# Kernel optimization log

Measured on AMD Instinct MI355X. Metric: run time of the kernel, lower is better.

The kernel has to match this reference:

```python
import jax, jax.numpy as jnp
import numpy as np

B, D, L, O = 131072, 128, 4, 1  # batch, d_model, num_layers(depths), estimator out dim


def setup_inputs() -> dict:
    key = jax.random.key(0)
    k0, k1, k2, k3 = jax.random.split(key, 4)
    x = jax.random.normal(k0, (B, D), jnp.float32)
    Wr = jax.random.normal(k1, (D, L), jnp.float32) * (1.0 / np.sqrt(D))
    W_layers = jax.random.normal(k2, (L, 2 * D, D), jnp.float32) * (1.0 / np.sqrt(2 * D))
    b_layers = jnp.zeros((L, D), jnp.float32)
    W_est = jax.random.normal(k3, (L, D, O), jnp.float32) * (1.0 / np.sqrt(D))
    b_est = jnp.zeros((L, O), jnp.float32)
    return {"x": x, "Wr": Wr, "W_layers": W_layers, "b_layers": b_layers,
            "W_est": W_est, "b_est": b_est}


def reference(x, Wr, W_layers, b_layers, W_est, b_est):
    # Router on stop_gradient(inputs); ReLU gate -> genuinely sparse gates (>0 test).
    gates = jax.nn.relu(jax.lax.stop_gradient(x) @ Wr)  # [B, L]

    def compute(last_out, depth):
        # layer depth: Dense on [last_layer_output, init_input]
        cur = jax.nn.relu(
            jnp.concatenate([last_out, x], axis=-1) @ W_layers[depth] + b_layers[depth]
        )  # [B, D]
        preds = cur @ W_est[depth] + b_est[depth]  # estimator at this depth, [B, O]
        if depth == L - 1:
            return preds
        # SparseDispatcher2D over 2 experts (exit / enter). combine() is an
        # unsorted_segment_sum over tokens with gate > 0 (unweighted), which is
        # exactly a 0/1-mask sum per token -- dense, jit-friendly equivalent.
        mask_exit = (gates[:, depth] > 0.0).astype(cur.dtype)[:, None]
        mask_enter = (jnp.sum(gates[:, depth + 1:], axis=1) > 0.0).astype(cur.dtype)[:, None]
        return mask_exit * preds + mask_enter * compute(cur, depth + 1)

    return compute(x, 0)
```

## Files before the change

### kernel.cpp

```cpp
#include <hip/hip_runtime.h>
#include <cstddef>

typedef float f4 __attribute__((ext_vector_type(4)));
typedef __bf16 bf16x8 __attribute__((ext_vector_type(8)));
typedef __bf16 bf16x4 __attribute__((ext_vector_type(4)));
typedef float f32x16 __attribute__((ext_vector_type(16)));

constexpr int D_ = 128;
constexpr int LAYERS = 4;
constexpr int BM = 128;
constexpr int NT = 256;
constexpr int ROWB = 512;

__device__ __forceinline__ int swz(int row, int woff) {
    return row * ROWB + (woff ^ ((row & 15) << 4));
}

__global__ void prep(const float* __restrict__ Wl, __bf16* __restrict__ wt2) {
    int idx = blockIdx.x * 256 + threadIdx.x;
    int j = idx & 7, lane = (idx >> 3) & 63, kc = (idx >> 9) & 15,
        nf = (idx >> 13) & 3, d = idx >> 15;
    int n  = nf * 32 + (lane & 31);
    int ks = kc * 16 + (lane >> 5) * 8 + j;
    float v;
    if (d == 0)
        v = (ks < 128) ? 0.f
                       : (Wl[(size_t)(ks - 128) * D_ + n] + Wl[(size_t)ks * D_ + n]);
    else
        v = Wl[(size_t)d * 2 * D_ * D_ + (size_t)ks * D_ + n];
    wt2[idx] = (__bf16)v;
}

__global__ __launch_bounds__(NT, 2)
void moe_fwd(const float* __restrict__ x, const float* __restrict__ Wr,
             const __bf16* __restrict__ wt2, const float* __restrict__ bl,
             const float* __restrict__ We, const float* __restrict__ be,
             float* __restrict__ out)
{
    __shared__ char Ab[BM * ROWB];
    __shared__ float PR[2][BM];
    __shared__ float CSM[BM][4];

    const int t    = threadIdx.x;
    const int m0   = blockIdx.x * BM;
    const int lane = t & 63, w = t >> 6;
    const int nw   = w >> 1;
    const int tw   = w & 1;
    const int lo5  = lane & 31, hi = lane >> 5;
    const int hi16 = hi * 16;
    const int tok0 = tw * 64 + lo5, tok1 = tok0 + 32;
    const int grp  = t >> 4, il = t & 15;

    f4 wrv[8];
    #pragma unroll
    for (int j = 0; j < 8; ++j)
        wrv[j] = *(const f4*)(Wr + (il * 8 + j) * 4);

    #pragma unroll
    for (int i = 0; i < 8; ++i) {
        const int row = i * 16 + grp;
        const f4* gx = (const f4*)(x + (size_t)(m0 + row) * D_ + il * 8);
        f4 lo = gx[0], hp = gx[1];
        bf16x8 v;
        v[0] = (__bf16)lo[0]; v[1] = (__bf16)lo[1]; v[2] = (__bf16)lo[2]; v[3] = (__bf16)lo[3];
        v[4] = (__bf16)hp[0]; v[5] = (__bf16)hp[1]; v[6] = (__bf16)hp[2]; v[7] = (__bf16)hp[3];
        *(bf16x8*)(Ab + swz(row, 256 + il * 16)) = v;

        double a0 = 0, a1 = 0, a2 = 0, a3 = 0;
        #pragma unroll
        for (int j = 0; j < 4; ++j) {
            double xv = (double)lo[j];
            a0 += xv * (double)wrv[j][0]; a1 += xv * (double)wrv[j][1];
            a2 += xv * (double)wrv[j][2]; a3 += xv * (double)wrv[j][3];
        }
        #pragma unroll
        for (int j = 0; j < 4; ++j) {
            double xv = (double)hp[j];
            a0 += xv * (double)wrv[4 + j][0]; a1 += xv * (double)wrv[4 + j][1];
            a2 += xv * (double)wrv[4 + j][2]; a3 += xv * (double)wrv[4 + j][3];
        }
        #pragma unroll
        for (int s = 1; s < 16; s <<= 1) {
            a0 += __shfl_xor(a0, s, 16);
            a1 += __shfl_xor(a1, s, 16);
            a2 += __shfl_xor(a2, s, 16);
            a3 += __shfl_xor(a3, s, 16);
        }
        if (il == 0) {
            f4 c;
            c[0] = a0 > 0.0 ? 1.f : 0.f; c[1] = a1 > 0.0 ? 1.f : 0.f;
            c[2] = a2 > 0.0 ? 1.f : 0.f; c[3] = a3 > 0.0 ? 1.f : 0.f;
            *(f4*)(&CSM[row][0]) = c;
        }
    }

    float outc = 0.f;
    __syncthreads();

    #pragma unroll
    for (int d = 0; d < LAYERS; ++d) {
        const int kstart = (d == 0) ? 8 : 0;

        bf16x8 wf[2][16];
        {
            const __bf16* wb = wt2 + ((size_t)(d * 4 + nw * 2) * 16) * 512 + lane * 8;
            #pragma unroll
            for (int m = 0; m < 2; ++m)
                #pragma unroll
                for (int kc = 0; kc < 16; ++kc)
                    if (kc >= kstart)
                        wf[m][kc] = *(const bf16x8*)(wb + (size_t)(m * 16 + kc) * 512);
        }

        f32x16 acc[2][2];
        #pragma unroll
        for (int m = 0; m < 2; ++m)
            #pragma unroll
            for (int tf = 0; tf < 2; ++tf)
                #pragma unroll
                for (int j = 0; j < 16; ++j) acc[m][tf][j] = 0.f;

        #pragma unroll
        for (int ks = 0; ks < 16; ++ks) {
            if (ks < kstart) continue;
            int wo = ks * 32 + hi16;
            bf16x8 b0 = *(const bf16x8*)(Ab + swz(tok0, wo));
            bf16x8 b1 = *(const bf16x8*)(Ab + swz(tok1, wo));
            acc[0][0] = __builtin_amdgcn_mfma_f32_32x32x16_bf16(wf[0][ks], b0, acc[0][0], 0, 0, 0);
            acc[0][1] = __builtin_amdgcn_mfma_f32_32x32x16_bf16(wf[0][ks], b1, acc[0][1], 0, 0, 0);
            acc[1][0] = __builtin_amdgcn_mfma_f32_32x32x16_bf16(wf[1][ks], b0, acc[1][0], 0, 0, 0);
            acc[1][1] = __builtin_amdgcn_mfma_f32_32x32x16_bf16(wf[1][ks], b1, acc[1][1], 0, 0, 0);
        }
        __syncthreads();

        float p0 = 0.f, p1 = 0.f;
        #pragma unroll
        for (int m = 0; m < 2; ++m) {
            #pragma unroll
            for (int rg = 0; rg < 4; ++rg) {
                int nb = nw * 64 + m * 32 + rg * 8 + hi * 4;
                f4 bv = *(const f4*)(bl + d * D_ + nb);
                f4 ev = *(const f4*)(We + d * D_ + nb);
                #pragma unroll
                for (int tf = 0; tf < 2; ++tf) {
                    float c0 = fmaxf(acc[m][tf][rg * 4 + 0] + bv[0], 0.f);
                    float c1 = fmaxf(acc[m][tf][rg * 4 + 1] + bv[1], 0.f);
                    float c2 = fmaxf(acc[m][tf][rg * 4 + 2] + bv[2], 0.f);
                    float c3 = fmaxf(acc[m][tf][rg * 4 + 3] + bv[3], 0.f);
                    float pp = c0 * ev[0] + c1 * ev[1] + c2 * ev[2] + c3 * ev[3];
                    if (tf == 0) p0 += pp; else p1 += pp;
                    if (d < LAYERS - 1) {
                        bf16x4 cc;
                        cc[0] = (__bf16)c0; cc[1] = (__bf16)c1;
                        cc[2] = (__bf16)c2; cc[3] = (__bf16)c3;
                        int token = tw * 64 + tf * 32 + lo5;
                        *(bf16x4*)(Ab + swz(token, nb * 2)) = cc;
                    }
                }
            }
        }
        p0 += __shfl_xor(p0, 32, 64);
        p1 += __shfl_xor(p1, 32, 64);
        if (lane < 32) {
            PR[nw][tw * 64 + lo5]      = p0;
            PR[nw][tw * 64 + 32 + lo5] = p1;
        }
        __syncthreads();

        if (t < BM)
            outc += CSM[t][d] * (PR[0][t] + PR[1][t] + be[d]);
    }

    if (t < BM) out[m0 + t] = outc;
}

extern "C" void kernel_launch(void* const* d_in, const int* in_sizes, int n_in,
                              void* d_out, int out_size, void* d_ws, size_t ws_size,
                              hipStream_t stream) {
    const float* x  = (const float*)d_in[0];
    const float* Wr = (const float*)d_in[1];
    const float* Wl = (const float*)d_in[2];
    const float* bl = (const float*)d_in[3];
    const float* We = (const float*)d_in[4];
    const float* be = (const float*)d_in[5];
    float* out = (float*)d_out;
    __bf16* wt2 = (__bf16*)d_ws;
    const int B = in_sizes[0] / D_;

    prep<<<dim3(512), dim3(256), 0, stream>>>(Wl, wt2);
    moe_fwd<<<dim3(B / BM), dim3(NT), 0, stream>>>(x, Wr, wt2, bl, We, be, out);
}
```

Before: 56.37 us.

## Double block threads to eight waves, each owning one 32-wide output slice

Raises the block from 256 to 512 threads so each of eight waves computes one 32-column output fragment for 64 tokens, instead of two fragments per wave. Each wave now holds half the weight registers and half the accumulators, which lowers register pressure and allows more concurrent waves. The initial x load and router loop is split across twice as many threads, and the partial estimator sums are reduced over four slices instead of two. Trade-offs are more threads contending at each barrier and more redundant LDS reads of the token operand.

```diff
diff --git a/kernel.cpp b/kernel.cpp
--- a/kernel.cpp
+++ b/kernel.cpp
@@ -9,7 +9,7 @@
 constexpr int D_ = 128;
 constexpr int LAYERS = 4;
 constexpr int BM = 128;
-constexpr int NT = 256;
+constexpr int NT = 512;
 constexpr int ROWB = 512;
 
 __device__ __forceinline__ int swz(int row, int woff) {
@@ -31,20 +31,20 @@
     wt2[idx] = (__bf16)v;
 }
 
-__global__ __launch_bounds__(NT, 2)
+__global__ __launch_bounds__(NT, 4)
 void moe_fwd(const float* __restrict__ x, const float* __restrict__ Wr,
              const __bf16* __restrict__ wt2, const float* __restrict__ bl,
              const float* __restrict__ We, const float* __restrict__ be,
              float* __restrict__ out)
 {
     __shared__ char Ab[BM * ROWB];
-    __shared__ float PR[2][BM];
+    __shared__ float PR[4][BM];
     __shared__ float CSM[BM][4];
 
     const int t    = threadIdx.x;
     const int m0   = blockIdx.x * BM;
     const int lane = t & 63, w = t >> 6;
-    const int nw   = w >> 1;
+    const int nf   = w >> 1;
     const int tw   = w & 1;
     const int lo5  = lane & 31, hi = lane >> 5;
     const int hi16 = hi * 16;
@@ -57,8 +57,8 @@
         wrv[j] = *(const f4*)(Wr + (il * 8 + j) * 4);
 
     #pragma unroll
-    for (int i = 0; i < 8; ++i) {
-        const int row = i * 16 + grp;
+    for (int i = 0; i < 4; ++i) {
+        const int row = i * 32 + grp;
         const f4* gx = (const f4*)(x + (size_t)(m0 + row) * D_ + il * 8);
         f4 lo = gx[0], hp = gx[1];
         bf16x8 v;
@@ -101,24 +101,20 @@
     for (int d = 0; d < LAYERS; ++d) {
         const int kstart = (d == 0) ? 8 : 0;
 
-        bf16x8 wf[2][16];
+        bf16x8 wf[16];
         {
-            const __bf16* wb = wt2 + ((size_t)(d * 4 + nw * 2) * 16) * 512 + lane * 8;
+            const __bf16* wb = wt2 + ((size_t)(d * 4 + nf) * 16) * 512 + lane * 8;
             #pragma unroll
-            for (int m = 0; m < 2; ++m)
-                #pragma unroll
-                for (int kc = 0; kc < 16; ++kc)
-                    if (kc >= kstart)
-                        wf[m][kc] = *(const bf16x8*)(wb + (size_t)(m * 16 + kc) * 512);
+            for (int kc = 0; kc < 16; ++kc)
+                if (kc >= kstart)
+                    wf[kc] = *(const bf16x8*)(wb + (size_t)kc * 512);
         }
 
-        f32x16 acc[2][2];
+        f32x16 acc[2];
         #pragma unroll
-        for (int m = 0; m < 2; ++m)
+        for (int tf = 0; tf < 2; ++tf)
             #pragma unroll
-            for (int tf = 0; tf < 2; ++tf)
-                #pragma unroll
-                for (int j = 0; j < 16; ++j) acc[m][tf][j] = 0.f;
+            for (int j = 0; j < 16; ++j) acc[tf][j] = 0.f;
 
         #pragma unroll
         for (int ks = 0; ks < 16; ++ks) {
@@ -126,49 +122,44 @@
             int wo = ks * 32 + hi16;
             bf16x8 b0 = *(const bf16x8*)(Ab + swz(tok0, wo));
             bf16x8 b1 = *(const bf16x8*)(Ab + swz(tok1, wo));
-            acc[0][0] = __builtin_amdgcn_mfma_f32_32x32x16_bf16(wf[0][ks], b0, acc[0][0], 0, 0, 0);
-            acc[0][1] = __builtin_amdgcn_mfma_f32_32x32x16_bf16(wf[0][ks], b1, acc[0][1], 0, 0, 0);
-            acc[1][0] = __builtin_amdgcn_mfma_f32_32x32x16_bf16(wf[1][ks], b0, acc[1][0], 0, 0, 0);
-            acc[1][1] = __builtin_amdgcn_mfma_f32_32x32x16_bf16(wf[1][ks], b1, acc[1][1], 0, 0, 0);
+            acc[0] = __builtin_amdgcn_mfma_f32_32x32x16_bf16(wf[ks], b0, acc[0], 0, 0, 0);
+            acc[1] = __builtin_amdgcn_mfma_f32_32x32x16_bf16(wf[ks], b1, acc[1], 0, 0, 0);
         }
         __syncthreads();
 
         float p0 = 0.f, p1 = 0.f;
         #pragma unroll
-        for (int m = 0; m < 2; ++m) {
+        for (int rg = 0; rg < 4; ++rg) {
+            int nb = nf * 32 + rg * 8 + hi * 4;
+            f4 bv = *(const f4*)(bl + d * D_ + nb);
+            f4 ev = *(const f4*)(We + d * D_ + nb);
             #pragma unroll
-            for (int rg = 0; rg < 4; ++rg) {
-                int nb = nw * 64 + m * 32 + rg * 8 + hi * 4;
-                f4 bv = *(const f4*)(bl + d * D_ + nb);
-                f4 ev = *(const f4*)(We + d * D_ + nb);
-                #pragma unroll
-                for (int tf = 0; tf < 2; ++tf) {
-                    float c0 = fmaxf(acc[m][tf][rg * 4 + 0] + bv[0], 0.f);
-                    float c1 = fmaxf(acc[m][tf][rg * 4 + 1] + bv[1], 0.f);
-                    float c2 = fmaxf(acc[m][tf][rg * 4 + 2] + bv[2], 0.f);
-                    float c3 = fmaxf(acc[m][tf][rg * 4 + 3] + bv[3], 0.f);
-                    float pp = c0 * ev[0] + c1 * ev[1] + c2 * ev[2] + c3 * ev[3];
-                    if (tf == 0) p0 += pp; else p1 += pp;
-                    if (d < LAYERS - 1) {
-                        bf16x4 cc;
-                        cc[0] = (__bf16)c0; cc[1] = (__bf16)c1;
-                        cc[2] = (__bf16)c2; cc[3] = (__bf16)c3;
-                        int token = tw * 64 + tf * 32 + lo5;
-                        *(bf16x4*)(Ab + swz(token, nb * 2)) = cc;
-                    }
+            for (int tf = 0; tf < 2; ++tf) {
+                float c0 = fmaxf(acc[tf][rg * 4 + 0] + bv[0], 0.f);
+                float c1 = fmaxf(acc[tf][rg * 4 + 1] + bv[1], 0.f);
+                float c2 = fmaxf(acc[tf][rg * 4 + 2] + bv[2], 0.f);
+                float c3 = fmaxf(acc[tf][rg * 4 + 3] + bv[3], 0.f);
+                float pp = c0 * ev[0] + c1 * ev[1] + c2 * ev[2] + c3 * ev[3];
+                if (tf == 0) p0 += pp; else p1 += pp;
+                if (d < LAYERS - 1) {
+                    bf16x4 cc;
+                    cc[0] = (__bf16)c0; cc[1] = (__bf16)c1;
+                    cc[2] = (__bf16)c2; cc[3] = (__bf16)c3;
+                    int token = tw * 64 + tf * 32 + lo5;
+                    *(bf16x4*)(Ab + swz(token, nb * 2)) = cc;
                 }
             }
         }
         p0 += __shfl_xor(p0, 32, 64);
         p1 += __shfl_xor(p1, 32, 64);
         if (lane < 32) {
-            PR[nw][tw * 64 + lo5]      = p0;
-            PR[nw][tw * 64 + 32 + lo5] = p1;
+            PR[nf][tw * 64 + lo5]      = p0;
+            PR[nf][tw * 64 + 32 + lo5] = p1;
         }
         __syncthreads();
 
         if (t < BM)
-            outc += CSM[t][d] * (PR[0][t] + PR[1][t] + be[d]);
+            outc += CSM[t][d] * (PR[0][t] + PR[1][t] + PR[2][t] + PR[3][t] + be[d]);
     }
 
     if (t < BM) out[m0 + t] = outc;
```

After: 54.27 us. -3.7%, faster.

## Keep activations in registers across layers via permuted weight K-order

Applied to the files above, without the earlier changes.

Each wave now owns 32 tokens and all 128 output columns, so the layer output produced in MFMA accumulator layout is repacked directly into registers as the next layer's B operand. The prep kernel permutes the K rows of layers 1-3 so that the register layout matches, which removes the shared-memory activation buffer and most block barriers. Shared memory drops to the gate table and launch bounds rise to 3 blocks per SM for occupancy. In exchange each wave loads the full weight set per layer (four times more weight traffic per wave), and register pressure rises from holding x and previous-layer activations.

```diff
diff --git a/kernel.cpp b/kernel.cpp
--- a/kernel.cpp
+++ b/kernel.cpp
@@ -3,175 +3,152 @@
 
 typedef float f4 __attribute__((ext_vector_type(4)));
 typedef __bf16 bf16x8 __attribute__((ext_vector_type(8)));
-typedef __bf16 bf16x4 __attribute__((ext_vector_type(4)));
 typedef float f32x16 __attribute__((ext_vector_type(16)));
 
 constexpr int D_ = 128;
 constexpr int LAYERS = 4;
 constexpr int BM = 128;
 constexpr int NT = 256;
-constexpr int ROWB = 512;
-
-__device__ __forceinline__ int swz(int row, int woff) {
-    return row * ROWB + (woff ^ ((row & 15) << 4));
-}
 
 __global__ void prep(const float* __restrict__ Wl, __bf16* __restrict__ wt2) {
     int idx = blockIdx.x * 256 + threadIdx.x;
-    int j = idx & 7, lane = (idx >> 3) & 63, kc = (idx >> 9) & 15,
-        nf = (idx >> 13) & 3, d = idx >> 15;
-    int n  = nf * 32 + (lane & 31);
-    int ks = kc * 16 + (lane >> 5) * 8 + j;
+    int j = idx & 7, lane = (idx >> 3) & 63, f = (idx >> 9) & 15,
+        c = (idx >> 13) & 3, d = idx >> 15;
+    int n = c * 32 + (lane & 31);
+    int k = f * 16 + (lane >> 5) * 8 + j;
     float v;
-    if (d == 0)
-        v = (ks < 128) ? 0.f
-                       : (Wl[(size_t)(ks - 128) * D_ + n] + Wl[(size_t)ks * D_ + n]);
-    else
-        v = Wl[(size_t)d * 2 * D_ * D_ + (size_t)ks * D_ + n];
+    if (d == 0) {
+        v = (k < 128) ? 0.f
+                      : (Wl[(size_t)(k - 128) * D_ + n] + Wl[(size_t)k * D_ + n]);
+    } else {
+        int kl;
+        if (k < 128) {
+            int jj = k & 7, hh = (k >> 3) & 1, ff = (k >> 4) & 7;
+            kl = (ff >> 1) * 32 + ((ff & 1) * 2 + (jj >> 2)) * 8 + hh * 4 + (jj & 3);
+        } else {
+            kl = k;
+        }
+        v = Wl[(size_t)d * 2 * D_ * D_ + (size_t)kl * D_ + n];
+    }
     wt2[idx] = (__bf16)v;
 }
 
-__global__ __launch_bounds__(NT, 2)
+__global__ __launch_bounds__(NT, 3)
 void moe_fwd(const float* __restrict__ x, const float* __restrict__ Wr,
              const __bf16* __restrict__ wt2, const float* __restrict__ bl,
              const float* __restrict__ We, const float* __restrict__ be,
              float* __restrict__ out)
 {
-    __shared__ char Ab[BM * ROWB];
-    __shared__ float PR[2][BM];
     __shared__ float CSM[BM][4];
 
     const int t    = threadIdx.x;
     const int m0   = blockIdx.x * BM;
     const int lane = t & 63, w = t >> 6;
-    const int nw   = w >> 1;
-    const int tw   = w & 1;
     const int lo5  = lane & 31, hi = lane >> 5;
-    const int hi16 = hi * 16;
-    const int tok0 = tw * 64 + lo5, tok1 = tok0 + 32;
+    const int tok  = w * 32 + lo5;
     const int grp  = t >> 4, il = t & 15;
 
-    f4 wrv[8];
+    bf16x8 xb[8];
     #pragma unroll
-    for (int j = 0; j < 8; ++j)
-        wrv[j] = *(const f4*)(Wr + (il * 8 + j) * 4);
+    for (int fi = 0; fi < 8; ++fi) {
+        const f4* gx = (const f4*)(x + (size_t)(m0 + tok) * D_ + fi * 16 + hi * 8);
+        f4 a = gx[0], b = gx[1];
+        xb[fi][0] = (__bf16)a[0]; xb[fi][1] = (__bf16)a[1];
+        xb[fi][2] = (__bf16)a[2]; xb[fi][3] = (__bf16)a[3];
+        xb[fi][4] = (__bf16)b[0]; xb[fi][5] = (__bf16)b[1];
+        xb[fi][6] = (__bf16)b[2]; xb[fi][7] = (__bf16)b[3];
+    }
 
-    #pragma unroll
-    for (int i = 0; i < 8; ++i) {
-        const int row = i * 16 + grp;
-        const f4* gx = (const f4*)(x + (size_t)(m0 + row) * D_ + il * 8);
-        f4 lo = gx[0], hp = gx[1];
-        bf16x8 v;
-        v[0] = (__bf16)lo[0]; v[1] = (__bf16)lo[1]; v[2] = (__bf16)lo[2]; v[3] = (__bf16)lo[3];
-        v[4] = (__bf16)hp[0]; v[5] = (__bf16)hp[1]; v[6] = (__bf16)hp[2]; v[7] = (__bf16)hp[3];
-        *(bf16x8*)(Ab + swz(row, 256 + il * 16)) = v;
-
-        double a0 = 0, a1 = 0, a2 = 0, a3 = 0;
+    {
+        f4 wrv[8];
         #pragma unroll
-        for (int j = 0; j < 4; ++j) {
-            double xv = (double)lo[j];
-            a0 += xv * (double)wrv[j][0]; a1 += xv * (double)wrv[j][1];
-            a2 += xv * (double)wrv[j][2]; a3 += xv * (double)wrv[j][3];
-        }
+        for (int j = 0; j < 8; ++j)
+            wrv[j] = *(const f4*)(Wr + (il * 8 + j) * 4);
         #pragma unroll
-        for (int j = 0; j < 4; ++j) {
-            double xv = (double)hp[j];
-            a0 += xv * (double)wrv[4 + j][0]; a1 += xv * (double)wrv[4 + j][1];
-            a2 += xv * (double)wrv[4 + j][2]; a3 += xv * (double)wrv[4 + j][3];
-        }
-        #pragma unroll
-        for (int s = 1; s < 16; s <<= 1) {
-            a0 += __shfl_xor(a0, s, 16);
-            a1 += __shfl_xor(a1, s, 16);
-            a2 += __shfl_xor(a2, s, 16);
-            a3 += __shfl_xor(a3, s, 16);
-        }
-        if (il == 0) {
-            f4 c;
-            c[0] = a0 > 0.0 ? 1.f : 0.f; c[1] = a1 > 0.0 ? 1.f : 0.f;
-            c[2] = a2 > 0.0 ? 1.f : 0.f; c[3] = a3 > 0.0 ? 1.f : 0.f;
-            *(f4*)(&CSM[row][0]) = c;
+        for (int i = 0; i < 8; ++i) {
+            const int row = i * 16 + grp;
+            const f4* gx = (const f4*)(x + (size_t)(m0 + row) * D_ + il * 8);
+            f4 lo = gx[0], hp = gx[1];
+            double a0 = 0, a1 = 0, a2 = 0, a3 = 0;
+            #pragma unroll
+            for (int j = 0; j < 4; ++j) {
+                double xv = (double)lo[j];
+                a0 += xv * (double)wrv[j][0]; a1 += xv * (double)wrv[j][1];
+                a2 += xv * (double)wrv[j][2]; a3 += xv * (double)wrv[j][3];
+            }
+            #pragma unroll
+            for (int j = 0; j < 4; ++j) {
+                double xv = (double)hp[j];
+                a0 += xv * (double)wrv[4 + j][0]; a1 += xv * (double)wrv[4 + j][1];
+                a2 += xv * (double)wrv[4 + j][2]; a3 += xv * (double)wrv[4 + j][3];
+            }
+            #pragma unroll
+            for (int s = 1; s < 16; s <<= 1) {
+                a0 += __shfl_xor(a0, s, 16);
+                a1 += __shfl_xor(a1, s, 16);
+                a2 += __shfl_xor(a2, s, 16);
+                a3 += __shfl_xor(a3, s, 16);
+            }
+            if (il == 0) {
+                f4 c;
+                c[0] = a0 > 0.0 ? 1.f : 0.f; c[1] = a1 > 0.0 ? 1.f : 0.f;
+                c[2] = a2 > 0.0 ? 1.f : 0.f; c[3] = a3 > 0.0 ? 1.f : 0.f;
+                *(f4*)(&CSM[row][0]) = c;
+            }
         }
     }
+    __syncthreads();
+    f4 cfv = *(const f4*)(&CSM[tok][0]);
 
     float outc = 0.f;
-    __syncthreads();
+    bf16x8 pb[8];
 
     #pragma unroll
     for (int d = 0; d < LAYERS; ++d) {
-        const int kstart = (d == 0) ? 8 : 0;
+        f32x16 acc[4];
+        #pragma unroll
+        for (int c = 0; c < 4; ++c)
+            #pragma unroll
+            for (int j = 0; j < 16; ++j) acc[c][j] = 0.f;
 
-        bf16x8 wf[2][16];
-        {
-            const __bf16* wb = wt2 + ((size_t)(d * 4 + nw * 2) * 16) * 512 + lane * 8;
+        const __bf16* wb = wt2 + (size_t)(d * 4 * 16) * 512 + (size_t)lane * 8;
+        #pragma unroll
+        for (int c = 0; c < 4; ++c) {
+            bf16x8 wf[16];
             #pragma unroll
-            for (int m = 0; m < 2; ++m)
-                #pragma unroll
-                for (int kc = 0; kc < 16; ++kc)
-                    if (kc >= kstart)
-                        wf[m][kc] = *(const bf16x8*)(wb + (size_t)(m * 16 + kc) * 512);
+            for (int f = (d == 0 ? 8 : 0); f < 16; ++f)
+                wf[f] = *(const bf16x8*)(wb + (size_t)(c * 16 + f) * 512);
+            #pragma unroll
+            for (int f = (d == 0 ? 8 : 0); f < 16; ++f)
+                acc[c] = __builtin_amdgcn_mfma_f32_32x32x16_bf16(
+                             wf[f], (f < 8) ? pb[f] : xb[f - 8], acc[c], 0, 0, 0);
         }
 
-        f32x16 acc[2][2];
+        float p = 0.f;
         #pragma unroll
-        for (int m = 0; m < 2; ++m)
-            #pragma unroll
-            for (int tf = 0; tf < 2; ++tf)
-                #pragma unroll
-                for (int j = 0; j < 16; ++j) acc[m][tf][j] = 0.f;
-
-        #pragma unroll
-        for (int ks = 0; ks < 16; ++ks) {
-            if (ks < kstart) continue;
-            int wo = ks * 32 + hi16;
-            bf16x8 b0 = *(const bf16x8*)(Ab + swz(tok0, wo));
-            bf16x8 b1 = *(const bf16x8*)(Ab + swz(tok1, wo));
-            acc[0][0] = __builtin_amdgcn_mfma_f32_32x32x16_bf16(wf[0][ks], b0, acc[0][0], 0, 0, 0);
-            acc[0][1] = __builtin_amdgcn_mfma_f32_32x32x16_bf16(wf[0][ks], b1, acc[0][1], 0, 0, 0);
-            acc[1][0] = __builtin_amdgcn_mfma_f32_32x32x16_bf16(wf[1][ks], b0, acc[1][0], 0, 0, 0);
-            acc[1][1] = __builtin_amdgcn_mfma_f32_32x32x16_bf16(wf[1][ks], b1, acc[1][1], 0, 0, 0);
-        }
-        __syncthreads();
-
-        float p0 = 0.f, p1 = 0.f;
-        #pragma unroll
-        for (int m = 0; m < 2; ++m) {
+        for (int c = 0; c < 4; ++c) {
             #pragma unroll
             for (int rg = 0; rg < 4; ++rg) {
-                int nb = nw * 64 + m * 32 + rg * 8 + hi * 4;
+                int nb = c * 32 + rg * 8 + hi * 4;
                 f4 bv = *(const f4*)(bl + d * D_ + nb);
                 f4 ev = *(const f4*)(We + d * D_ + nb);
-                #pragma unroll
-                for (int tf = 0; tf < 2; ++tf) {
-                    float c0 = fmaxf(acc[m][tf][rg * 4 + 0] + bv[0], 0.f);
-                    float c1 = fmaxf(acc[m][tf][rg * 4 + 1] + bv[1], 0.f);
-                    float c2 = fmaxf(acc[m][tf][rg * 4 + 2] + bv[2], 0.f);
-                    float c3 = fmaxf(acc[m][tf][rg * 4 + 3] + bv[3], 0.f);
-                    float pp = c0 * ev[0] + c1 * ev[1] + c2 * ev[2] + c3 * ev[3];
-                    if (tf == 0) p0 += pp; else p1 += pp;
-                    if (d < LAYERS - 1) {
-                        bf16x4 cc;
-                        cc[0] = (__bf16)c0; cc[1] = (__bf16)c1;
-                        cc[2] = (__bf16)c2; cc[3] = (__bf16)c3;
-                        int token = tw * 64 + tf * 32 + lo5;
-                        *(bf16x4*)(Ab + swz(token, nb * 2)) = cc;
-                    }
+                float c0 = fmaxf(acc[c][rg * 4 + 0] + bv[0], 0.f);
+                float c1 = fmaxf(acc[c][rg * 4 + 1] + bv[1], 0.f);
+                float c2 = fmaxf(acc[c][rg * 4 + 2] + bv[2], 0.f);
+                float c3 = fmaxf(acc[c][rg * 4 + 3] + bv[3], 0.f);
+                p += c0 * ev[0] + c1 * ev[1] + c2 * ev[2] + c3 * ev[3];
+                if (d < LAYERS - 1) {
+                    const int f = c * 2 + (rg >> 1), jb = (rg & 1) * 4;
+                    pb[f][jb + 0] = (__bf16)c0; pb[f][jb + 1] = (__bf16)c1;
+                    pb[f][jb + 2] = (__bf16)c2; pb[f][jb + 3] = (__bf16)c3;
                 }
             }
         }
-        p0 += __shfl_xor(p0, 32, 64);
-        p1 += __shfl_xor(p1, 32, 64);
-        if (lane < 32) {
-            PR[nw][tw * 64 + lo5]      = p0;
-            PR[nw][tw * 64 + 32 + lo5] = p1;
-        }
-        __syncthreads();
-
-        if (t < BM)
-            outc += CSM[t][d] * (PR[0][t] + PR[1][t] + be[d]);
+        p += __shfl_xor(p, 32, 64);
+        if (lane < 32) outc += cfv[d] * (p + be[d]);
     }
 
-    if (t < BM) out[m0 + t] = outc;
+    if (lane < 32) out[m0 + tok] = outc;
 }
 
 extern "C" void kernel_launch(void* const* d_in, const int* in_sizes, int n_in,
```

Measured after the change: 96.62 us. 71.4% more time.
